# Performance work log

Hardware: AMD Instinct MI355X
Metric: run time of the kernel (lower is better)

## Reference

```python
import jax, jax.numpy as jnp
import numpy as np

N, C, F, E = 32768, 256, 1024, 16
TOP_K = 2


def setup_inputs() -> dict:
    key = jax.random.key(0)
    k_x, k_gw, k_w1, k_w2 = jax.random.split(key, 4)
    x = jax.random.normal(k_x, (N, C), dtype=jnp.float32)
    gate_W = jax.random.normal(k_gw, (E, C), dtype=jnp.float32) * 0.01  # nn.init.normal_(std=0.01)
    gate_b = jnp.zeros((E,), dtype=jnp.float32)
    W1 = jax.random.normal(k_w1, (E, C, F), dtype=jnp.float32) * 0.02
    b1 = jnp.zeros((E, F), dtype=jnp.float32)
    W2 = jax.random.normal(k_w2, (E, F, C), dtype=jnp.float32) * 0.02
    b2 = jnp.zeros((E, C), dtype=jnp.float32)
    return {"x": x, "gate_W": gate_W, "gate_b": gate_b,
            "W1": W1, "b1": b1, "W2": W2, "b2": b2}


def reference(x, gate_W, gate_b, W1, b1, W2, b2):
    # Gating (eval mode: no gaussian noise)
    gate_logits = x @ gate_W.T + gate_b                       # [N, E]
    gate_probs = jax.nn.softmax(gate_logits, axis=-1)
    gate_entropy = -(gate_probs * jnp.log(gate_probs + 1e-8)).sum(axis=-1).mean()

    topk_val, topk_idx = jax.lax.top_k(gate_logits, TOP_K)   # [N, K]
    gate_weights = jax.nn.softmax(topk_val, axis=-1)          # softmax over the top-k logits

    # Dense all-expert FFN compute (matches the torch stack over experts)
    h = jax.nn.relu(jnp.einsum('nc,ecf->enf', x, W1) + b1[:, None, :])   # [E, N, F]
    expert_outputs = jnp.einsum('enf,efc->enc', h, W2) + b2[:, None, :]  # [E, N, C]

    # Gather top-k expert outputs per token and combine
    eo = jnp.transpose(expert_outputs, (1, 0, 2))             # [N, E, C]
    selected = jnp.take_along_axis(eo, topk_idx[:, :, None], axis=1)  # [N, K, C]
    out = (gate_weights[:, :, None] * selected).sum(axis=1)  # [N, C]

    # default args: return_gate=False, return_entropy=True
    return out, gate_entropy
```

## Files before the change

### kernel.cpp

```cpp
#include <hip/hip_runtime.h>
#include <hip/hip_bf16.h>
#include <math.h>

#define N_TOK 32768
#define C_DIM 256
#define F_DIM 1024
#define E_NUM 16
#define TILE_R 128
#define NCH 16
#define NBLK 544

typedef unsigned short u16;
typedef unsigned int u32;
typedef __attribute__((ext_vector_type(4))) u16 u16x4;
typedef __attribute__((ext_vector_type(8))) u16 u16x8;
typedef __attribute__((ext_vector_type(8))) short bf16x8;
typedef __attribute__((ext_vector_type(4))) u32 u32x4;
typedef __attribute__((ext_vector_type(16))) float f32x16;

#define AS1 __attribute__((address_space(1)))
#define AS3 __attribute__((address_space(3)))

__device__ __forceinline__ void gload16(const void* g, void* lds) {
    __builtin_amdgcn_global_load_lds((const AS1 u32*)(uintptr_t)g,
                                     (AS3 u32*)(u32)(uintptr_t)lds, 16, 0, 0);
}

__device__ __forceinline__ u16 f2bf(float f) {
    union { float f; u32 u; } v; v.f = f;
    u32 r = v.u + 0x7fffu + ((v.u >> 16) & 1u);
    return (u16)(r >> 16);
}

__device__ __forceinline__ float bf2f(u16 b) {
    union { u32 u; float f; } v; v.u = ((u32)b) << 16;
    return v.f;
}


__global__ __launch_bounds__(256) void gate_kernel(
    const float* __restrict__ x, const float* __restrict__ gW,
    const float* __restrict__ gb, float* __restrict__ ent_out,
    int* __restrict__ tidx, float* __restrict__ tw, int* __restrict__ counts,
    u16* __restrict__ xb)
{
    __shared__ float gws[E_NUM * C_DIM];
    __shared__ float gbs[E_NUM];
    __shared__ float went[4];
    __shared__ int lc[E_NUM];
    int tid = threadIdx.x;

    for (int i = tid; i < E_NUM * C_DIM / 4; i += 256)
        ((float4*)gws)[i] = ((const float4*)gW)[i];
    if (tid < E_NUM) { gbs[tid] = gb[tid]; lc[tid] = 0; }
    __syncthreads();

    int tok = tid >> 2, q = tid & 3;
    int n = blockIdx.x * 64 + tok;
    const float* xr = x + (size_t)n * C_DIM;

    float4 xv[16];
    #pragma unroll
    for (int j = 0; j < 16; j++)
        xv[j] = *(const float4*)(xr + j * 16 + q * 4);

    #pragma unroll
    for (int j = 0; j < 16; j++) {
        u16x4 o;
        o[0] = f2bf(xv[j].x); o[1] = f2bf(xv[j].y);
        o[2] = f2bf(xv[j].z); o[3] = f2bf(xv[j].w);
        *(u16x4*)(xb + (size_t)n * C_DIM + j * 16 + q * 4) = o;
    }

    float lg[E_NUM];
    #pragma unroll
    for (int e = 0; e < E_NUM; e++) lg[e] = 0.f;
    #pragma unroll
    for (int j = 0; j < 16; j++) {
        #pragma unroll
        for (int e = 0; e < E_NUM; e++) {
            float4 g = *(const float4*)(gws + e * C_DIM + j * 16 + q * 4);
            lg[e] += xv[j].x * g.x + xv[j].y * g.y + xv[j].z * g.z + xv[j].w * g.w;
        }
    }
    #pragma unroll
    for (int e = 0; e < E_NUM; e++) {
        lg[e] += __shfl_xor(lg[e], 1);
        lg[e] += __shfl_xor(lg[e], 2);
        lg[e] += gbs[e];
    }

    float m = lg[0];
    #pragma unroll
    for (int e = 1; e < E_NUM; e++) m = fmaxf(m, lg[e]);
    float s = 0.f, ex[E_NUM];
    #pragma unroll
    for (int e = 0; e < E_NUM; e++) { ex[e] = __expf(lg[e] - m); s += ex[e]; }
    float inv = 1.f / s;
    float ent = 0.f;
    #pragma unroll
    for (int e = 0; e < E_NUM; e++) {
        float p = ex[e] * inv;
        ent -= p * logf(p + 1e-8f);
    }

    float v0 = -1e30f, v1 = -1e30f;
    int i0 = 0, i1 = 0;
    #pragma unroll
    for (int e = 0; e < E_NUM; e++) {
        float l = lg[e];
        if (l > v0) { v1 = v0; i1 = i0; v0 = l; i0 = e; }
        else if (l > v1) { v1 = l; i1 = e; }
    }
    if (q == 0) {
        float w1e = __expf(v1 - v0);
        float z = 1.f + w1e;
        tidx[2 * n] = i0; tidx[2 * n + 1] = i1;
        tw[2 * n] = 1.f / z; tw[2 * n + 1] = w1e / z;
        atomicAdd(&lc[i0], 1);
        atomicAdd(&lc[i1], 1);
    }

    float v = ent;
    for (int off = 32; off > 0; off >>= 1) v += __shfl_down(v, off);
    int wid = tid >> 6, lane = tid & 63;
    if (lane == 0) went[wid] = v;
    __syncthreads();
    if (tid == 0)
        atomicAdd(ent_out, (went[0] + went[1] + went[2] + went[3]) * (1.0f / (4.0f * N_TOK)));
    if (tid < E_NUM && lc[tid]) atomicAdd(&counts[tid], lc[tid]);
}

__global__ void prefix_kernel(const int* __restrict__ counts,
                              int* __restrict__ offs, int* __restrict__ tp)
{
    if (threadIdx.x == 0 && blockIdx.x == 0) {
        int o = 0, t = 0;
        offs[0] = 0; tp[0] = 0;
        for (int e = 0; e < E_NUM; e++) {
            o += counts[e];
            t += (counts[e] + TILE_R - 1) / TILE_R;
            offs[e + 1] = o;
            tp[e + 1] = t;
        }
    }
}

__global__ __launch_bounds__(256) void scatter_kernel(
    const int* __restrict__ tidx, const float* __restrict__ tw,
    const int* __restrict__ offs, int* __restrict__ fill,
    int* __restrict__ tok, float* __restrict__ wgt, int* __restrict__ pairpos)
{
    __shared__ int lc[E_NUM], lbase[E_NUM];
    int tid = threadIdx.x;
    if (tid < E_NUM) lc[tid] = 0;
    __syncthreads();
    int n = blockIdx.x * 256 + tid;
    int e0 = tidx[2 * n], e1 = tidx[2 * n + 1];
    int r0 = atomicAdd(&lc[e0], 1);
    int r1 = atomicAdd(&lc[e1], 1);
    __syncthreads();
    if (tid < E_NUM) lbase[tid] = offs[tid] + atomicAdd(&fill[tid], lc[tid]);
    __syncthreads();
    int p0 = lbase[e0] + r0, p1 = lbase[e1] + r1;
    tok[p0] = n; wgt[p0] = tw[2 * n];     pairpos[2 * n] = p0;
    tok[p1] = n; wgt[p1] = tw[2 * n + 1]; pairpos[2 * n + 1] = p1;
}

__global__ __launch_bounds__(256) void tcvt_kernel(
    const float* __restrict__ src, u16* __restrict__ dst, int R, int Cc)
{
    __shared__ float t[64][65];
    int e = blockIdx.x;
    int r0 = blockIdx.y << 6, c0 = blockIdx.z << 6;
    const float* s = src + (size_t)e * R * Cc;
    u16* d = dst + (size_t)e * R * Cc;
    int tid = threadIdx.x;
    int rr = tid >> 4, cc = (tid & 15) << 2;
    #pragma unroll
    for (int it = 0; it < 4; it++) {
        float4 v = *(const float4*)(s + (size_t)(r0 + rr + it * 16) * Cc + c0 + cc);
        t[rr + it * 16][cc] = v.x; t[rr + it * 16][cc + 1] = v.y;
        t[rr + it * 16][cc + 2] = v.z; t[rr + it * 16][cc + 3] = v.w;
    }
    __syncthreads();
    int cr = tid >> 3, rq = (tid & 7) << 3;
    #pragma unroll
    for (int it = 0; it < 2; it++) {
        int c = cr + it * 32;
        u16x8 o;
        #pragma unroll
        for (int j = 0; j < 8; j++) o[j] = f2bf(t[rq + j][c]);
        *(u16x8*)(d + (size_t)(c0 + c) * R + r0 + rq) = o;
    }
}

#define HS_OFF  131072
#define B1S_OFF 147456

template <int MODE>
__global__ __launch_bounds__(512, 2) void ffn_mfma(
    const u16* __restrict__ xb, const u16* __restrict__ w1t,
    const u16* __restrict__ w2t, const float* __restrict__ b1,
    const float* __restrict__ b2, const int* __restrict__ tok,
    const float* __restrict__ wgt, const int* __restrict__ offs,
    const int* __restrict__ tp, u16* __restrict__ ybuf,
    float* __restrict__ out)
{
    __shared__ __align__(1024) char smem[152576];
    int* s_tok = (int*)(smem + 151552);
    float* s_w = (float*)(smem + 152064);
    float* b1s = (float*)(smem + B1S_OFF);

    int idx = blockIdx.x;
    int b = (idx & 7) * (NBLK / 8) + (idx >> 3);
    if (b >= tp[E_NUM]) return;
    int e = 0;
    while (b >= tp[e + 1]) e++;
    int base = offs[e] + ((b - tp[e]) << 7);
    int rows = offs[e + 1] - base; if (rows > TILE_R) rows = TILE_R;

    int tid = threadIdx.x;
    int lane = tid & 63, wid = tid >> 6;
    int hi = lane >> 5;
    int wr = wid >> 1, wc = wid & 1;

    const u16* w1e = w1t + (size_t)e * (F_DIM * C_DIM);
    const u16* w2e = w2t + (size_t)e * (C_DIM * F_DIM);
    const float* b1e = b1 + e * F_DIM;
    const float* b2e = b2 + e * C_DIM;

    if (tid < TILE_R) {
        int src = (tid < rows) ? base + tid : base;
        s_tok[tid] = tok[src];
        s_w[tid] = (tid < rows) ? wgt[src] : 0.f;
    }
    if (tid < 256) ((float4*)b1s)[tid] = ((const float4*)b1e)[tid];
    __syncthreads();

    #pragma unroll
    for (int i = 0; i < 8; i++) {
        int idx2 = (wid << 3) + i;
        int row = ((idx2 >> 4) << 5) + (lane & 31);
        gload16(xb + ((size_t)s_tok[row] << 8) + ((idx2 & 15) << 4) + (hi << 3),
                smem + (idx2 << 10));
    }
    __syncthreads();

    bf16x8 xr[16];
    #pragma unroll
    for (int ks = 0; ks < 16; ks++)
        xr[ks] = *(const bf16x8*)(smem + (wr << 14) + (ks << 10) + (lane << 4));
    __syncthreads();

    u32x4 sg[8];
    #pragma unroll
    for (int i = 0; i < 4; i++) {
        int idx2 = (wid << 2) + i;
        int f = ((idx2 >> 4) << 5) + (lane & 31);
        sg[i] = *(const u32x4*)(w1e + ((size_t)f << 8) + ((idx2 & 15) << 4) + (hi << 3));
        int c = ((idx2 >> 2) << 5) + (lane & 31);
        sg[4 + i] = *(const u32x4*)(w2e + ((size_t)c << 10) + ((idx2 & 3) << 4) + (hi << 3));
    }
    #pragma unroll
    for (int i = 0; i < 4; i++) {
        int idx2 = (wid << 2) + i;
        *(u32x4*)(smem + (idx2 << 10) + (lane << 4)) = sg[i];
        *(u32x4*)(smem + 32768 + (idx2 << 10) + (lane << 4)) = sg[4 + i];
    }

    f32x16 acc2[4];
    #pragma unroll
    for (int ct = 0; ct < 4; ct++) acc2[ct] = (f32x16)(0.0f);

    for (int ch = 0; ch < NCH; ch++) {
        int cur = ch & 1;
        const char* cbuf = smem + (cur << 16);

        asm volatile("s_waitcnt lgkmcnt(0)" ::: "memory");
        __builtin_amdgcn_s_barrier();
        __builtin_amdgcn_sched_barrier(0);

        {
            int chn = ch + 1; if (chn == NCH) chn = NCH - 1;
            #pragma unroll
            for (int i = 0; i < 4; i++) {
                int idx2 = (wid << 2) + i;
                int f = (chn << 6) + ((idx2 >> 4) << 5) + (lane & 31);
                sg[i] = *(const u32x4*)(w1e + ((size_t)f << 8) + ((idx2 & 15) << 4) + (hi << 3));
                int c = ((idx2 >> 2) << 5) + (lane & 31);
                sg[4 + i] = *(const u32x4*)(w2e + ((size_t)c << 10) + (chn << 6) + ((idx2 & 3) << 4) + (hi << 3));
            }
        }

        const char* w1b = cbuf + (wc << 14) + (lane << 4);
        f32x16 acc1a = (f32x16)(0.0f), acc1b = (f32x16)(0.0f);
        __builtin_amdgcn_s_setprio(1);
        #pragma unroll
        for (int ks = 0; ks < 8; ks++) {
            bf16x8 a0 = *(const bf16x8*)(w1b + ((2 * ks) << 10));
            bf16x8 a1 = *(const bf16x8*)(w1b + ((2 * ks + 1) << 10));
            acc1a = __builtin_amdgcn_mfma_f32_32x32x16_bf16(a0, xr[2 * ks], acc1a, 0, 0, 0);
            acc1b = __builtin_amdgcn_mfma_f32_32x32x16_bf16(a1, xr[2 * ks + 1], acc1b, 0, 0, 0);
        }
        __builtin_amdgcn_s_setprio(0);

        float h[16];
        #pragma unroll
        for (int r = 0; r < 16; r++) {
            int fl = (wc << 5) + (r & 3) + ((r >> 2) << 3) + (hi << 2);
            h[r] = fmaxf(acc1a[r] + acc1b[r] + b1s[(ch << 6) + fl], 0.f);
        }
        u32 w[8];
        #pragma unroll
        for (int t = 0; t < 8; t++)
            asm("v_cvt_pk_bf16_f32 %0, %1, %2" : "=v"(w[t]) : "v"(h[2 * t]), "v"(h[2 * t + 1]));
        asm volatile("v_permlane32_swap_b32 %0, %1" : "+v"(w[0]), "+v"(w[2]));
        asm volatile("v_permlane32_swap_b32 %0, %1" : "+v"(w[1]), "+v"(w[3]));
        asm volatile("v_permlane32_swap_b32 %0, %1" : "+v"(w[4]), "+v"(w[6]));
        asm volatile("v_permlane32_swap_b32 %0, %1" : "+v"(w[5]), "+v"(w[7]));
        union { u32x4 u; bf16x8 v; } fr0, fr1, pr0, pr1;
        fr0.u = (u32x4){w[0], w[1], w[2], w[3]};
        fr1.u = (u32x4){w[4], w[5], w[6], w[7]};

        *(u32x4*)(smem + HS_OFF + (wr << 12) + ((wc << 1) << 10) + (lane << 4)) = fr0.u;
        *(u32x4*)(smem + HS_OFF + (wr << 12) + (((wc << 1) + 1) << 10) + (lane << 4)) = fr1.u;

        asm volatile("s_waitcnt lgkmcnt(0)" ::: "memory");
        __builtin_amdgcn_s_barrier();
        __builtin_amdgcn_sched_barrier(0);

        {
            char* nbuf = smem + ((cur ^ 1) << 16);
            #pragma unroll
            for (int i = 0; i < 4; i++) {
                int idx2 = (wid << 2) + i;
                *(u32x4*)(nbuf + (idx2 << 10) + (lane << 4)) = sg[i];
                *(u32x4*)(nbuf + 32768 + (idx2 << 10) + (lane << 4)) = sg[4 + i];
            }
        }

        pr0.u = *(const u32x4*)(smem + HS_OFF + (wr << 12) + (((wc ^ 1) << 1) << 10) + (lane << 4));
        pr1.u = *(const u32x4*)(smem + HS_OFF + (wr << 12) + ((((wc ^ 1) << 1) + 1) << 10) + (lane << 4));

        const char* w2b = cbuf + 32768 + (wc << 14) + (lane << 4);
        bf16x8 bh0, bh1, bh2, bh3;
        if (wc == 0) { bh0 = fr0.v; bh1 = fr1.v; bh2 = pr0.v; bh3 = pr1.v; }
        else         { bh0 = pr0.v; bh1 = pr1.v; bh2 = fr0.v; bh3 = fr1.v; }

        __builtin_amdgcn_s_setprio(1);
        #define P2_STEP(BH, S2)                                               \
            _Pragma("unroll")                                                 \
            for (int ctl = 0; ctl < 4; ctl++) {                               \
                bf16x8 a = *(const bf16x8*)(w2b + (ctl << 12) + ((S2) << 10));\
                acc2[ctl] = __builtin_amdgcn_mfma_f32_32x32x16_bf16(a, BH, acc2[ctl], 0, 0, 0); \
            }
        P2_STEP(bh0, 0)
        P2_STEP(bh1, 1)
        P2_STEP(bh2, 2)
        P2_STEP(bh3, 3)
        #undef P2_STEP
        __builtin_amdgcn_s_setprio(0);
    }

    int m = (wr << 5) + (lane & 31);
    if (m < rows) {
        if (MODE == 0) {
            u16* yr = ybuf + ((size_t)(base + m) << 8) + (wc << 7);
            #pragma unroll
            for (int ctl = 0; ctl < 4; ctl++) {
                #pragma unroll
                for (int rq = 0; rq < 4; rq++) {
                    int c = (ctl << 5) + (rq << 3) + (hi << 2);
                    u16x4 o;
                    o[0] = f2bf(acc2[ctl][4 * rq]);
                    o[1] = f2bf(acc2[ctl][4 * rq + 1]);
                    o[2] = f2bf(acc2[ctl][4 * rq + 2]);
                    o[3] = f2bf(acc2[ctl][4 * rq + 3]);
                    *(u16x4*)(yr + c) = o;
                }
            }
        } else {
            float wgt_m = s_w[m];
            float* orow = out + ((size_t)s_tok[m] << 8) + (wc << 7);
            const float* b2w = b2e + (wc << 7);
            #pragma unroll
            for (int ctl = 0; ctl < 4; ctl++) {
                #pragma unroll
                for (int rq = 0; rq < 4; rq++) {
                    int c = (ctl << 5) + (rq << 3) + (hi << 2);
                    #pragma unroll
                    for (int l = 0; l < 4; l++)
                        atomicAdd(&orow[c + l],
                                  wgt_m * (acc2[ctl][4 * rq + l] + b2w[c + l]));
                }
            }
        }
    }
}

__global__ __launch_bounds__(256) void combine_kernel(
    const u16* __restrict__ ybuf, const int* __restrict__ tidx,
    const float* __restrict__ tw, const int* __restrict__ pairpos,
    const float* __restrict__ b2, float* __restrict__ out)
{
    int idx = blockIdx.x * 256 + threadIdx.x;
    int n = idx >> 6;
    int q = (idx & 63) << 2;
    int e0 = tidx[2 * n], e1 = tidx[2 * n + 1];
    float w0 = tw[2 * n], w1 = tw[2 * n + 1];
    int p0 = pairpos[2 * n], p1 = pairpos[2 * n + 1];
    u16x4 y0 = *(const u16x4*)(ybuf + ((size_t)p0 << 8) + q);
    u16x4 y1 = *(const u16x4*)(ybuf + ((size_t)p1 << 8) + q);
    float4 c0 = *(const float4*)(b2 + (e0 << 8) + q);
    float4 c1 = *(const float4*)(b2 + (e1 << 8) + q);
    float4 o;
    o.x = w0 * (bf2f(y0[0]) + c0.x) + w1 * (bf2f(y1[0]) + c1.x);
    o.y = w0 * (bf2f(y0[1]) + c0.y) + w1 * (bf2f(y1[1]) + c1.y);
    o.z = w0 * (bf2f(y0[2]) + c0.z) + w1 * (bf2f(y1[2]) + c1.z);
    o.w = w0 * (bf2f(y0[3]) + c0.w) + w1 * (bf2f(y1[3]) + c1.w);
    *(float4*)(out + ((size_t)n << 8) + q) = o;
}

extern "C" void kernel_launch(void* const* d_in, const int* in_sizes, int n_in,
                              void* d_out, int out_size, void* d_ws, size_t ws_size,
                              hipStream_t stream)
{
    const float* x   = (const float*)d_in[0];
    const float* gW  = (const float*)d_in[1];
    const float* gb  = (const float*)d_in[2];
    const float* W1  = (const float*)d_in[3];
    const float* b1  = (const float*)d_in[4];
    const float* W2  = (const float*)d_in[5];
    const float* b2  = (const float*)d_in[6];
    float* out = (float*)d_out;

    char* ws = (char*)d_ws;
    int*   topk_idx = (int*)(ws + 0);
    float* topk_w   = (float*)(ws + 262144);
    int*   tok      = (int*)(ws + 524288);
    float* wgt      = (float*)(ws + 786432);
    int*   pairpos  = (int*)(ws + 1048576);
    int*   counts   = (int*)(ws + 1310720);
    int*   fill     = (int*)(ws + 1310784);
    int*   offs     = (int*)(ws + 1310848);
    int*   tp       = (int*)(ws + 1310916);

    const size_t XB_OFF  = 2097152;
    const size_t W1T_OFF = 18874368;
    const size_t W2T_OFF = 27262976;
    const size_t Y_OFF   = 35651584;
    const size_t WS_FULL = Y_OFF + (size_t)2 * N_TOK * C_DIM * 2;

    u16* xb  = (u16*)(ws + XB_OFF);
    u16* w1t = (u16*)(ws + W1T_OFF);
    u16* w2t = (u16*)(ws + W2T_OFF);
    u16* ybuf = (u16*)(ws + Y_OFF);

    int mode = (ws_size >= WS_FULL) ? 0 : 1;

    float* ent_out = out + (size_t)N_TOK * C_DIM;

    if (mode == 0) {
        hipMemsetAsync(ent_out, 0, sizeof(float), stream);
    } else {
        hipMemsetAsync(d_out, 0, (size_t)(N_TOK * C_DIM + 1) * sizeof(float), stream);
    }
    hipMemsetAsync(counts, 0, 2 * E_NUM * sizeof(int), stream);

    gate_kernel<<<N_TOK / 64, 256, 0, stream>>>(x, gW, gb, ent_out,
                                                topk_idx, topk_w, counts, xb);
    prefix_kernel<<<1, 64, 0, stream>>>(counts, offs, tp);
    scatter_kernel<<<N_TOK / 256, 256, 0, stream>>>(topk_idx, topk_w, offs,
                                                    fill, tok, wgt, pairpos);
    tcvt_kernel<<<dim3(E_NUM, C_DIM / 64, F_DIM / 64), 256, 0, stream>>>(W1, w1t, C_DIM, F_DIM);
    tcvt_kernel<<<dim3(E_NUM, F_DIM / 64, C_DIM / 64), 256, 0, stream>>>(W2, w2t, F_DIM, C_DIM);

    if (mode == 0) {
        ffn_mfma<0><<<NBLK, 512, 0, stream>>>(xb, w1t, w2t, b1, b2, tok, wgt,
                                              offs, tp, ybuf, out);
        combine_kernel<<<N_TOK * 64 / 256, 256, 0, stream>>>(ybuf, topk_idx,
                                                             topk_w, pairpos, b2, out);
    } else {
        ffn_mfma<1><<<NBLK, 512, 0, stream>>>(xb, w1t, w2t, b1, b2, tok, wgt,
                                              offs, tp, ybuf, out);
    }
}
```

Measured before the change: 212.2 us.

## Shrink FFN tile to 64 rows with 4 waves and remove h exchange barrier

The grouped expert FFN kernel moves from 128-row tiles with 8 waves to 64-row tiles with 4 waves. F is processed in 32-wide chunks, so each wave computes its whole h slice locally and the LDS exchange of h between wave pairs, along with its second barrier, goes away. Weight staging becomes two chunks deep (register prefetch of ch+2 while storing ch+1), and the bias load is vectorised. Each weight tile is now reused across half as many tokens, which doubles the weight traffic per token. In exchange it gives more blocks, lower LDS use and one barrier per chunk instead of two.

```diff
diff --git a/kernel.cpp b/kernel.cpp
--- a/kernel.cpp
+++ b/kernel.cpp
@@ -6,9 +6,9 @@
 #define C_DIM 256
 #define F_DIM 1024
 #define E_NUM 16
-#define TILE_R 128
-#define NCH 16
-#define NBLK 544
+#define TILE_R 64
+#define NCH 32
+#define NBLK 1040
 
 typedef unsigned short u16;
 typedef unsigned int u32;
@@ -195,11 +195,10 @@
     }
 }
 
-#define HS_OFF  131072
-#define B1S_OFF 147456
+#define B1S_OFF 65536
 
 template <int MODE>
-__global__ __launch_bounds__(512, 2) void ffn_mfma(
+__global__ __launch_bounds__(256, 2) void ffn_mfma(
     const u16* __restrict__ xb, const u16* __restrict__ w1t,
     const u16* __restrict__ w2t, const float* __restrict__ b1,
     const float* __restrict__ b2, const int* __restrict__ tok,
@@ -207,17 +206,17 @@
     const int* __restrict__ tp, u16* __restrict__ ybuf,
     float* __restrict__ out)
 {
-    __shared__ __align__(1024) char smem[152576];
-    int* s_tok = (int*)(smem + 151552);
-    float* s_w = (float*)(smem + 152064);
+    __shared__ __align__(1024) char smem[70144];
+    int* s_tok = (int*)(smem + 69632);
+    float* s_w = (float*)(smem + 69888);
     float* b1s = (float*)(smem + B1S_OFF);
 
-    int idx = blockIdx.x;
-    int b = (idx & 7) * (NBLK / 8) + (idx >> 3);
+    int bidx = blockIdx.x;
+    int b = (bidx & 7) * (NBLK / 8) + (bidx >> 3);
     if (b >= tp[E_NUM]) return;
     int e = 0;
     while (b >= tp[e + 1]) e++;
-    int base = offs[e] + ((b - tp[e]) << 7);
+    int base = offs[e] + ((b - tp[e]) << 6);
     int rows = offs[e + 1] - base; if (rows > TILE_R) rows = TILE_R;
 
     int tid = threadIdx.x;
@@ -235,15 +234,15 @@
         s_tok[tid] = tok[src];
         s_w[tid] = (tid < rows) ? wgt[src] : 0.f;
     }
-    if (tid < 256) ((float4*)b1s)[tid] = ((const float4*)b1e)[tid];
+    ((float4*)b1s)[tid] = ((const float4*)b1e)[tid];
     __syncthreads();
 
     #pragma unroll
     for (int i = 0; i < 8; i++) {
-        int idx2 = (wid << 3) + i;
-        int row = ((idx2 >> 4) << 5) + (lane & 31);
-        gload16(xb + ((size_t)s_tok[row] << 8) + ((idx2 & 15) << 4) + (hi << 3),
-                smem + (idx2 << 10));
+        int idx = (wid << 3) + i;
+        int row = ((idx >> 4) << 5) + (lane & 31);
+        gload16(xb + ((size_t)s_tok[row] << 8) + ((idx & 15) << 4) + (hi << 3),
+                smem + (idx << 10));
     }
     __syncthreads();
 
@@ -256,17 +255,25 @@
     u32x4 sg[8];
     #pragma unroll
     for (int i = 0; i < 4; i++) {
-        int idx2 = (wid << 2) + i;
-        int f = ((idx2 >> 4) << 5) + (lane & 31);
-        sg[i] = *(const u32x4*)(w1e + ((size_t)f << 8) + ((idx2 & 15) << 4) + (hi << 3));
-        int c = ((idx2 >> 2) << 5) + (lane & 31);
-        sg[4 + i] = *(const u32x4*)(w2e + ((size_t)c << 10) + ((idx2 & 3) << 4) + (hi << 3));
+        int fid = (wid << 2) + i;
+        sg[i] = *(const u32x4*)(w1e + (size_t)(lane & 31) * 256 + (fid << 4) + (hi << 3));
+        int swc = fid >> 3, ctl = (fid >> 1) & 3, s2 = fid & 1;
+        int c = (swc << 7) + (ctl << 5) + (lane & 31);
+        sg[4 + i] = *(const u32x4*)(w2e + (size_t)c * 1024 + (s2 << 4) + (hi << 3));
     }
     #pragma unroll
     for (int i = 0; i < 4; i++) {
-        int idx2 = (wid << 2) + i;
-        *(u32x4*)(smem + (idx2 << 10) + (lane << 4)) = sg[i];
-        *(u32x4*)(smem + 32768 + (idx2 << 10) + (lane << 4)) = sg[4 + i];
+        int fid = (wid << 2) + i;
+        *(u32x4*)(smem + (fid << 10) + (lane << 4)) = sg[i];
+        *(u32x4*)(smem + 16384 + (fid << 10) + (lane << 4)) = sg[4 + i];
+    }
+    #pragma unroll
+    for (int i = 0; i < 4; i++) {
+        int fid = (wid << 2) + i;
+        sg[i] = *(const u32x4*)(w1e + (size_t)((1 << 5) + (lane & 31)) * 256 + (fid << 4) + (hi << 3));
+        int swc = fid >> 3, ctl = (fid >> 1) & 3, s2 = fid & 1;
+        int c = (swc << 7) + (ctl << 5) + (lane & 31);
+        sg[4 + i] = *(const u32x4*)(w2e + (size_t)c * 1024 + (1 << 5) + (s2 << 4) + (hi << 3));
     }
 
     f32x16 acc2[4];
@@ -275,25 +282,31 @@
 
     for (int ch = 0; ch < NCH; ch++) {
         int cur = ch & 1;
-        const char* cbuf = smem + (cur << 16);
+        const char* cbuf = smem + (cur << 15);
 
         asm volatile("s_waitcnt lgkmcnt(0)" ::: "memory");
         __builtin_amdgcn_s_barrier();
-        __builtin_amdgcn_sched_barrier(0);
 
         {
-            int chn = ch + 1; if (chn == NCH) chn = NCH - 1;
+            char* nbuf = smem + ((cur ^ 1) << 15);
             #pragma unroll
             for (int i = 0; i < 4; i++) {
-                int idx2 = (wid << 2) + i;
-                int f = (chn << 6) + ((idx2 >> 4) << 5) + (lane & 31);
-                sg[i] = *(const u32x4*)(w1e + ((size_t)f << 8) + ((idx2 & 15) << 4) + (hi << 3));
-                int c = ((idx2 >> 2) << 5) + (lane & 31);
-                sg[4 + i] = *(const u32x4*)(w2e + ((size_t)c << 10) + (chn << 6) + ((idx2 & 3) << 4) + (hi << 3));
+                int fid = (wid << 2) + i;
+                *(u32x4*)(nbuf + (fid << 10) + (lane << 4)) = sg[i];
+                *(u32x4*)(nbuf + 16384 + (fid << 10) + (lane << 4)) = sg[4 + i];
             }
-        }
-
-        const char* w1b = cbuf + (wc << 14) + (lane << 4);
+            int chn = ch + 2; if (chn > NCH - 1) chn = NCH - 1;
+            #pragma unroll
+            for (int i = 0; i < 4; i++) {
+                int fid = (wid << 2) + i;
+                sg[i] = *(const u32x4*)(w1e + (size_t)((chn << 5) + (lane & 31)) * 256 + (fid << 4) + (hi << 3));
+                int swc = fid >> 3, ctl = (fid >> 1) & 3, s2 = fid & 1;
+                int c = (swc << 7) + (ctl << 5) + (lane & 31);
+                sg[4 + i] = *(const u32x4*)(w2e + (size_t)c * 1024 + (chn << 5) + (s2 << 4) + (hi << 3));
+            }
+        }
+
+        const char* w1b = cbuf + (lane << 4);
         f32x16 acc1a = (f32x16)(0.0f), acc1b = (f32x16)(0.0f);
         __builtin_amdgcn_s_setprio(1);
         #pragma unroll
@@ -305,12 +318,16 @@
         }
         __builtin_amdgcn_s_setprio(0);
 
+        float4 bv0 = *(const float4*)(b1s + (ch << 5) + (hi << 2));
+        float4 bv1 = *(const float4*)(b1s + (ch << 5) + (hi << 2) + 8);
+        float4 bv2 = *(const float4*)(b1s + (ch << 5) + (hi << 2) + 16);
+        float4 bv3 = *(const float4*)(b1s + (ch << 5) + (hi << 2) + 24);
+        float bb[16] = {bv0.x, bv0.y, bv0.z, bv0.w, bv1.x, bv1.y, bv1.z, bv1.w,
+                        bv2.x, bv2.y, bv2.z, bv2.w, bv3.x, bv3.y, bv3.z, bv3.w};
         float h[16];
         #pragma unroll
-        for (int r = 0; r < 16; r++) {
-            int fl = (wc << 5) + (r & 3) + ((r >> 2) << 3) + (hi << 2);
-            h[r] = fmaxf(acc1a[r] + acc1b[r] + b1s[(ch << 6) + fl], 0.f);
-        }
+        for (int r = 0; r < 16; r++)
+            h[r] = fmaxf(acc1a[r] + acc1b[r] + bb[r], 0.f);
         u32 w[8];
         #pragma unroll
         for (int t = 0; t < 8; t++)
@@ -319,47 +336,19 @@
         asm volatile("v_permlane32_swap_b32 %0, %1" : "+v"(w[1]), "+v"(w[3]));
         asm volatile("v_permlane32_swap_b32 %0, %1" : "+v"(w[4]), "+v"(w[6]));
         asm volatile("v_permlane32_swap_b32 %0, %1" : "+v"(w[5]), "+v"(w[7]));
-        union { u32x4 u; bf16x8 v; } fr0, fr1, pr0, pr1;
+        union { u32x4 u; bf16x8 v; } fr0, fr1;
         fr0.u = (u32x4){w[0], w[1], w[2], w[3]};
         fr1.u = (u32x4){w[4], w[5], w[6], w[7]};
 
-        *(u32x4*)(smem + HS_OFF + (wr << 12) + ((wc << 1) << 10) + (lane << 4)) = fr0.u;
-        *(u32x4*)(smem + HS_OFF + (wr << 12) + (((wc << 1) + 1) << 10) + (lane << 4)) = fr1.u;
-
-        asm volatile("s_waitcnt lgkmcnt(0)" ::: "memory");
-        __builtin_amdgcn_s_barrier();
-        __builtin_amdgcn_sched_barrier(0);
-
-        {
-            char* nbuf = smem + ((cur ^ 1) << 16);
-            #pragma unroll
-            for (int i = 0; i < 4; i++) {
-                int idx2 = (wid << 2) + i;
-                *(u32x4*)(nbuf + (idx2 << 10) + (lane << 4)) = sg[i];
-                *(u32x4*)(nbuf + 32768 + (idx2 << 10) + (lane << 4)) = sg[4 + i];
-            }
-        }
-
-        pr0.u = *(const u32x4*)(smem + HS_OFF + (wr << 12) + (((wc ^ 1) << 1) << 10) + (lane << 4));
-        pr1.u = *(const u32x4*)(smem + HS_OFF + (wr << 12) + ((((wc ^ 1) << 1) + 1) << 10) + (lane << 4));
-
-        const char* w2b = cbuf + 32768 + (wc << 14) + (lane << 4);
-        bf16x8 bh0, bh1, bh2, bh3;
-        if (wc == 0) { bh0 = fr0.v; bh1 = fr1.v; bh2 = pr0.v; bh3 = pr1.v; }
-        else         { bh0 = pr0.v; bh1 = pr1.v; bh2 = fr0.v; bh3 = fr1.v; }
-
+        const char* w2b = cbuf + 16384 + (wc << 13) + (lane << 4);
         __builtin_amdgcn_s_setprio(1);
-        #define P2_STEP(BH, S2)                                               \
-            _Pragma("unroll")                                                 \
-            for (int ctl = 0; ctl < 4; ctl++) {                               \
-                bf16x8 a = *(const bf16x8*)(w2b + (ctl << 12) + ((S2) << 10));\
-                acc2[ctl] = __builtin_amdgcn_mfma_f32_32x32x16_bf16(a, BH, acc2[ctl], 0, 0, 0); \
-            }
-        P2_STEP(bh0, 0)
-        P2_STEP(bh1, 1)
-        P2_STEP(bh2, 2)
-        P2_STEP(bh3, 3)
-        #undef P2_STEP
+        #pragma unroll
+        for (int ctl = 0; ctl < 4; ctl++) {
+            bf16x8 a0 = *(const bf16x8*)(w2b + (ctl << 11));
+            bf16x8 a1 = *(const bf16x8*)(w2b + (ctl << 11) + 1024);
+            acc2[ctl] = __builtin_amdgcn_mfma_f32_32x32x16_bf16(a0, fr0.v, acc2[ctl], 0, 0, 0);
+            acc2[ctl] = __builtin_amdgcn_mfma_f32_32x32x16_bf16(a1, fr1.v, acc2[ctl], 0, 0, 0);
+        }
         __builtin_amdgcn_s_setprio(0);
     }
 
@@ -477,12 +466,12 @@
     tcvt_kernel<<<dim3(E_NUM, F_DIM / 64, C_DIM / 64), 256, 0, stream>>>(W2, w2t, F_DIM, C_DIM);
 
     if (mode == 0) {
-        ffn_mfma<0><<<NBLK, 512, 0, stream>>>(xb, w1t, w2t, b1, b2, tok, wgt,
+        ffn_mfma<0><<<NBLK, 256, 0, stream>>>(xb, w1t, w2t, b1, b2, tok, wgt,
                                               offs, tp, ybuf, out);
         combine_kernel<<<N_TOK * 64 / 256, 256, 0, stream>>>(ybuf, topk_idx,
                                                              topk_w, pairpos, b2, out);
     } else {
-        ffn_mfma<1><<<NBLK, 512, 0, stream>>>(xb, w1t, w2t, b1, b2, tok, wgt,
+        ffn_mfma<1><<<NBLK, 256, 0, stream>>>(xb, w1t, w2t, b1, b2, tok, wgt,
                                               offs, tp, ybuf, out);
     }
 }
```

Result: slower. 232.3 us (+9.5%).

## Pre-swizzle expert weights into MFMA fragment layout and stage via async LDS loads

Applied to the files above, without the earlier changes.

The weight-conversion kernels now write W1 and W2 in bf16, already arranged in the per-lane MFMA fragment order. The FFN kernel can then copy each chunk straight into LDS with global_load_lds, replacing the register round-trip that staged the next chunk through VGPRs. Half the waves load W1 and half load W2, with vmcnt waits and a barrier at the end of each chunk, and the s_setprio hints are removed. This frees registers and removes the separate LDS store phase. The cost is a full vmcnt drain and an extra barrier every iteration, which may expose load latency.

```diff
diff --git a/kernel.cpp b/kernel.cpp
--- a/kernel.cpp
+++ b/kernel.cpp
@@ -167,41 +167,83 @@
     tok[p1] = n; wgt[p1] = tw[2 * n + 1]; pairpos[2 * n + 1] = p1;
 }
 
-__global__ __launch_bounds__(256) void tcvt_kernel(
-    const float* __restrict__ src, u16* __restrict__ dst, int R, int Cc)
-{
-    __shared__ float t[64][65];
-    int e = blockIdx.x;
-    int r0 = blockIdx.y << 6, c0 = blockIdx.z << 6;
-    const float* s = src + (size_t)e * R * Cc;
-    u16* d = dst + (size_t)e * R * Cc;
+__global__ __launch_bounds__(256) void tcvt_w1f(
+    const float* __restrict__ W1, u16* __restrict__ w1f)
+{
+    __shared__ float t[256][33];
+    int e = blockIdx.x, ft = blockIdx.y;
     int tid = threadIdx.x;
-    int rr = tid >> 4, cc = (tid & 15) << 2;
-    #pragma unroll
-    for (int it = 0; it < 4; it++) {
-        float4 v = *(const float4*)(s + (size_t)(r0 + rr + it * 16) * Cc + c0 + cc);
-        t[rr + it * 16][cc] = v.x; t[rr + it * 16][cc + 1] = v.y;
-        t[rr + it * 16][cc + 2] = v.z; t[rr + it * 16][cc + 3] = v.w;
-    }
-    __syncthreads();
-    int cr = tid >> 3, rq = (tid & 7) << 3;
-    #pragma unroll
-    for (int it = 0; it < 2; it++) {
-        int c = cr + it * 32;
+    const float* src = W1 + ((size_t)e * C_DIM) * F_DIM + (size_t)tid * F_DIM + ft * 32;
+    #pragma unroll
+    for (int j = 0; j < 8; j++) {
+        float4 v = *(const float4*)(src + j * 4);
+        t[tid][j * 4] = v.x; t[tid][j * 4 + 1] = v.y;
+        t[tid][j * 4 + 2] = v.z; t[tid][j * 4 + 3] = v.w;
+    }
+    __syncthreads();
+    int l = tid & 63, ksq = tid >> 6;
+    #pragma unroll
+    for (int p = 0; p < 4; p++) {
+        int ks = ksq * 4 + p;
+        int c0 = ks * 16 + (l >> 5) * 8;
         u16x8 o;
         #pragma unroll
-        for (int j = 0; j < 8; j++) o[j] = f2bf(t[rq + j][c]);
-        *(u16x8*)(d + (size_t)(c0 + c) * R + r0 + rq) = o;
-    }
-}
-
-#define HS_OFF  131072
-#define B1S_OFF 147456
+        for (int j = 0; j < 8; j++) o[j] = f2bf(t[c0 + j][l & 31]);
+        *(u16x8*)(w1f + ((size_t)((e * 32 + ft) * 16 + ks)) * 512 + l * 8) = o;
+    }
+}
+
+__global__ __launch_bounds__(256) void tcvt_w2f(
+    const float* __restrict__ W2, u16* __restrict__ w2f)
+{
+    __shared__ float t[256][33];
+    int e = blockIdx.x, ct = blockIdx.y, fq = blockIdx.z;
+    int tid = threadIdx.x;
+    const float* src = W2 + ((size_t)e * F_DIM + fq * 256 + tid) * C_DIM + ct * 32;
+    #pragma unroll
+    for (int j = 0; j < 8; j++) {
+        float4 v = *(const float4*)(src + j * 4);
+        t[tid][j * 4] = v.x; t[tid][j * 4 + 1] = v.y;
+        t[tid][j * 4 + 2] = v.z; t[tid][j * 4 + 3] = v.w;
+    }
+    __syncthreads();
+    int l = tid & 63, kq = tid >> 6;
+    #pragma unroll
+    for (int p = 0; p < 4; p++) {
+        int kfl = kq * 4 + p;
+        int f0 = kfl * 16 + (l >> 5) * 8;
+        u16x8 o;
+        #pragma unroll
+        for (int j = 0; j < 8; j++) o[j] = f2bf(t[f0 + j][l & 31]);
+        *(u16x8*)(w2f + ((size_t)((e * 8 + ct) * 64 + fq * 16 + kfl)) * 512 + l * 8) = o;
+    }
+}
+
+#define HS_OFF  135168
+#define B1S_OFF 131072
+
+#define STAGE_CHUNK(CHN, NBUF)                                                \
+    if (wid < 4) {                                                            \
+        _Pragma("unroll")                                                     \
+        for (int i = 0; i < 8; i++) {                                         \
+            int fid = (wid << 3) + i;                                         \
+            gload16(w1fe + (((size_t)((CHN) << 5) + fid) << 9) + (lane << 3), \
+                    (NBUF) + (fid << 10));                                    \
+        }                                                                     \
+    } else {                                                                  \
+        _Pragma("unroll")                                                     \
+        for (int i = 0; i < 8; i++) {                                         \
+            int g = ((wid - 4) << 3) + i;                                     \
+            int ct = g >> 2, kfl = g & 3;                                     \
+            gload16(w2fe + (((size_t)(ct << 6) + ((CHN) << 2) + kfl) << 9) + (lane << 3), \
+                    (NBUF) + 32768 + (g << 10));                              \
+        }                                                                     \
+    }
 
 template <int MODE>
 __global__ __launch_bounds__(512, 2) void ffn_mfma(
-    const u16* __restrict__ xb, const u16* __restrict__ w1t,
-    const u16* __restrict__ w2t, const float* __restrict__ b1,
+    const u16* __restrict__ xb, const u16* __restrict__ w1f,
+    const u16* __restrict__ w2f, const float* __restrict__ b1,
     const float* __restrict__ b2, const int* __restrict__ tok,
     const float* __restrict__ wgt, const int* __restrict__ offs,
     const int* __restrict__ tp, u16* __restrict__ ybuf,
@@ -212,8 +254,8 @@
     float* s_w = (float*)(smem + 152064);
     float* b1s = (float*)(smem + B1S_OFF);
 
-    int idx = blockIdx.x;
-    int b = (idx & 7) * (NBLK / 8) + (idx >> 3);
+    int bidx = blockIdx.x;
+    int b = (bidx & 7) * (NBLK / 8) + (bidx >> 3);
     if (b >= tp[E_NUM]) return;
     int e = 0;
     while (b >= tp[e + 1]) e++;
@@ -225,8 +267,8 @@
     int hi = lane >> 5;
     int wr = wid >> 1, wc = wid & 1;
 
-    const u16* w1e = w1t + (size_t)e * (F_DIM * C_DIM);
-    const u16* w2e = w2t + (size_t)e * (C_DIM * F_DIM);
+    const u16* w1fe = w1f + ((size_t)e << 9) * 512;
+    const u16* w2fe = w2f + ((size_t)e << 9) * 512;
     const float* b1e = b1 + e * F_DIM;
     const float* b2e = b2 + e * C_DIM;
 
@@ -245,6 +287,7 @@
         gload16(xb + ((size_t)s_tok[row] << 8) + ((idx2 & 15) << 4) + (hi << 3),
                 smem + (idx2 << 10));
     }
+    asm volatile("s_waitcnt vmcnt(0)" ::: "memory");
     __syncthreads();
 
     bf16x8 xr[16];
@@ -253,21 +296,9 @@
         xr[ks] = *(const bf16x8*)(smem + (wr << 14) + (ks << 10) + (lane << 4));
     __syncthreads();
 
-    u32x4 sg[8];
-    #pragma unroll
-    for (int i = 0; i < 4; i++) {
-        int idx2 = (wid << 2) + i;
-        int f = ((idx2 >> 4) << 5) + (lane & 31);
-        sg[i] = *(const u32x4*)(w1e + ((size_t)f << 8) + ((idx2 & 15) << 4) + (hi << 3));
-        int c = ((idx2 >> 2) << 5) + (lane & 31);
-        sg[4 + i] = *(const u32x4*)(w2e + ((size_t)c << 10) + ((idx2 & 3) << 4) + (hi << 3));
-    }
-    #pragma unroll
-    for (int i = 0; i < 4; i++) {
-        int idx2 = (wid << 2) + i;
-        *(u32x4*)(smem + (idx2 << 10) + (lane << 4)) = sg[i];
-        *(u32x4*)(smem + 32768 + (idx2 << 10) + (lane << 4)) = sg[4 + i];
-    }
+    STAGE_CHUNK(0, smem)
+    asm volatile("s_waitcnt vmcnt(0)" ::: "memory");
+    __syncthreads();
 
     f32x16 acc2[4];
     #pragma unroll
@@ -277,25 +308,13 @@
         int cur = ch & 1;
         const char* cbuf = smem + (cur << 16);
 
-        asm volatile("s_waitcnt lgkmcnt(0)" ::: "memory");
-        __builtin_amdgcn_s_barrier();
-        __builtin_amdgcn_sched_barrier(0);
-
-        {
-            int chn = ch + 1; if (chn == NCH) chn = NCH - 1;
-            #pragma unroll
-            for (int i = 0; i < 4; i++) {
-                int idx2 = (wid << 2) + i;
-                int f = (chn << 6) + ((idx2 >> 4) << 5) + (lane & 31);
-                sg[i] = *(const u32x4*)(w1e + ((size_t)f << 8) + ((idx2 & 15) << 4) + (hi << 3));
-                int c = ((idx2 >> 2) << 5) + (lane & 31);
-                sg[4 + i] = *(const u32x4*)(w2e + ((size_t)c << 10) + (chn << 6) + ((idx2 & 3) << 4) + (hi << 3));
-            }
+        if (ch + 1 < NCH) {
+            char* nbuf = smem + ((cur ^ 1) << 16);
+            STAGE_CHUNK(ch + 1, nbuf)
         }
 
         const char* w1b = cbuf + (wc << 14) + (lane << 4);
         f32x16 acc1a = (f32x16)(0.0f), acc1b = (f32x16)(0.0f);
-        __builtin_amdgcn_s_setprio(1);
         #pragma unroll
         for (int ks = 0; ks < 8; ks++) {
             bf16x8 a0 = *(const bf16x8*)(w1b + ((2 * ks) << 10));
@@ -303,7 +322,6 @@
             acc1a = __builtin_amdgcn_mfma_f32_32x32x16_bf16(a0, xr[2 * ks], acc1a, 0, 0, 0);
             acc1b = __builtin_amdgcn_mfma_f32_32x32x16_bf16(a1, xr[2 * ks + 1], acc1b, 0, 0, 0);
         }
-        __builtin_amdgcn_s_setprio(0);
 
         float h[16];
         #pragma unroll
@@ -330,16 +348,6 @@
         __builtin_amdgcn_s_barrier();
         __builtin_amdgcn_sched_barrier(0);
 
-        {
-            char* nbuf = smem + ((cur ^ 1) << 16);
-            #pragma unroll
-            for (int i = 0; i < 4; i++) {
-                int idx2 = (wid << 2) + i;
-                *(u32x4*)(nbuf + (idx2 << 10) + (lane << 4)) = sg[i];
-                *(u32x4*)(nbuf + 32768 + (idx2 << 10) + (lane << 4)) = sg[4 + i];
-            }
-        }
-
         pr0.u = *(const u32x4*)(smem + HS_OFF + (wr << 12) + (((wc ^ 1) << 1) << 10) + (lane << 4));
         pr1.u = *(const u32x4*)(smem + HS_OFF + (wr << 12) + ((((wc ^ 1) << 1) + 1) << 10) + (lane << 4));
 
@@ -348,7 +356,6 @@
         if (wc == 0) { bh0 = fr0.v; bh1 = fr1.v; bh2 = pr0.v; bh3 = pr1.v; }
         else         { bh0 = pr0.v; bh1 = pr1.v; bh2 = fr0.v; bh3 = fr1.v; }
 
-        __builtin_amdgcn_s_setprio(1);
         #define P2_STEP(BH, S2)                                               \
             _Pragma("unroll")                                                 \
             for (int ctl = 0; ctl < 4; ctl++) {                               \
@@ -360,7 +367,10 @@
         P2_STEP(bh2, 2)
         P2_STEP(bh3, 3)
         #undef P2_STEP
-        __builtin_amdgcn_s_setprio(0);
+
+        asm volatile("s_waitcnt vmcnt(0) lgkmcnt(0)" ::: "memory");
+        __builtin_amdgcn_s_barrier();
+        __builtin_amdgcn_sched_barrier(0);
     }
 
     int m = (wr << 5) + (lane & 31);
@@ -390,9 +400,9 @@
                 for (int rq = 0; rq < 4; rq++) {
                     int c = (ctl << 5) + (rq << 3) + (hi << 2);
                     #pragma unroll
-                    for (int l = 0; l < 4; l++)
-                        atomicAdd(&orow[c + l],
-                                  wgt_m * (acc2[ctl][4 * rq + l] + b2w[c + l]));
+                    for (int l2 = 0; l2 < 4; l2++)
+                        atomicAdd(&orow[c + l2],
+                                  wgt_m * (acc2[ctl][4 * rq + l2] + b2w[c + l2]));
                 }
             }
         }
@@ -447,14 +457,14 @@
     int*   tp       = (int*)(ws + 1310916);
 
     const size_t XB_OFF  = 2097152;
-    const size_t W1T_OFF = 18874368;
-    const size_t W2T_OFF = 27262976;
+    const size_t W1F_OFF = 18874368;
+    const size_t W2F_OFF = 27262976;
     const size_t Y_OFF   = 35651584;
     const size_t WS_FULL = Y_OFF + (size_t)2 * N_TOK * C_DIM * 2;
 
     u16* xb  = (u16*)(ws + XB_OFF);
-    u16* w1t = (u16*)(ws + W1T_OFF);
-    u16* w2t = (u16*)(ws + W2T_OFF);
+    u16* w1f = (u16*)(ws + W1F_OFF);
+    u16* w2f = (u16*)(ws + W2F_OFF);
     u16* ybuf = (u16*)(ws + Y_OFF);
 
     int mode = (ws_size >= WS_FULL) ? 0 : 1;
@@ -473,16 +483,16 @@
     prefix_kernel<<<1, 64, 0, stream>>>(counts, offs, tp);
     scatter_kernel<<<N_TOK / 256, 256, 0, stream>>>(topk_idx, topk_w, offs,
                                                     fill, tok, wgt, pairpos);
-    tcvt_kernel<<<dim3(E_NUM, C_DIM / 64, F_DIM / 64), 256, 0, stream>>>(W1, w1t, C_DIM, F_DIM);
-    tcvt_kernel<<<dim3(E_NUM, F_DIM / 64, C_DIM / 64), 256, 0, stream>>>(W2, w2t, F_DIM, C_DIM);
+    tcvt_w1f<<<dim3(E_NUM, 32), 256, 0, stream>>>(W1, w1f);
+    tcvt_w2f<<<dim3(E_NUM, 8, 4), 256, 0, stream>>>(W2, w2f);
 
     if (mode == 0) {
-        ffn_mfma<0><<<NBLK, 512, 0, stream>>>(xb, w1t, w2t, b1, b2, tok, wgt,
+        ffn_mfma<0><<<NBLK, 512, 0, stream>>>(xb, w1f, w2f, b1, b2, tok, wgt,
                                               offs, tp, ybuf, out);
         combine_kernel<<<N_TOK * 64 / 256, 256, 0, stream>>>(ybuf, topk_idx,
                                                              topk_w, pairpos, b2, out);
     } else {
-        ffn_mfma<1><<<NBLK, 512, 0, stream>>>(xb, w1t, w2t, b1, b2, tok, wgt,
+        ffn_mfma<1><<<NBLK, 512, 0, stream>>>(xb, w1f, w2f, b1, b2, tok, wgt,
                                               offs, tp, ybuf, out);
     }
 }
```

New measurement: 183.5 us. -13.5%, faster.
